# Performance work log

Hardware: AMD Instinct MI355X
Metric: run time of the kernel (lower is better)

Reference implementation:

```python
import jax, jax.numpy as jnp
import numpy as np

# ---- config (mirrors AAModel init kwargs: ns=48, nv=10, sh_lmax=1) ----
N, E, NS, NV = 100000, 60000, 48, 10
SED, DED = 32, 32          # sigma / distance embedding dims
CUTOFF = 30.0              # GaussianSmearing(0, cutoff, DED)
SQ3 = float(np.sqrt(3.0))
W1_NUMEL = NS * NS + NS * NV                                   # 2784
# layer-2 fully-connected TP path weight offsets:
#   0e(x)0e->0e, 0e(x)1o->1o, 1o(x)0e->1o, 1o(x)1o->0e, 1o(x)1o->1e
O2 = [2304, 2784, 2884, 3364, 3464]


def _mlp2(x, W1, b1, W2, b2):
    return jax.nn.relu(x @ W1 + b1) @ W2 + b2


def _seg_mean(x, idx, n):
    s = jax.ops.segment_sum(x, idx, num_segments=n)
    cnt = jax.ops.segment_sum(jnp.ones(idx.shape, x.dtype), idx, num_segments=n)
    return s / jnp.maximum(cnt, 1.0).reshape((n,) + (1,) * (x.ndim - 1))


def _forward(pos, node_sigma_emb, node_s, edge_W1, edge_b1, edge_W2, edge_b2,
             fc1_W1, fc1_b1, fc1_W2, fc1_b2, fc2_W1, fc2_b1, fc2_W2, fc2_b2,
             edge_index):
    src, dst = edge_index[0], edge_index[1]
    vec = pos[dst] - pos[src]                          # [E,3]
    d = jnp.linalg.norm(vec, axis=-1)                  # [E]
    sh1 = SQ3 * vec / (d[:, None] + 1e-8)              # l=1 SH, component norm; sh0 == 1
    # Gaussian smearing of edge distances
    offsets = jnp.linspace(0.0, CUTOFF, DED)
    coeff = -0.5 / (offsets[1] - offsets[0]) ** 2
    demb = jnp.exp(coeff * (d[:, None] - offsets) ** 2)          # [E,DED]
    edge_emb = _mlp2(jnp.concatenate([node_sigma_emb[src], demb], -1),
                     edge_W1, edge_b1, edge_W2, edge_b2)         # [E,NS]

    # ---- conv layer 1:  ns x0e  (x)  1x0e+1x1o  ->  ns x0e + nv x1o ----
    xs = node_s[src]
    ea = jnp.concatenate([edge_emb, node_s[src], node_s[dst]], -1)   # [E,3*NS]
    w = _mlp2(ea, fc1_W1, fc1_b1, fc1_W2, fc1_b2)                    # [E,2784]
    w00 = w[:, :NS * NS].reshape(-1, NS, NS)
    w01 = w[:, NS * NS:].reshape(-1, NS, NV)
    inv = 1.0 / np.sqrt(NS)
    m_s = jnp.einsum('eio,ei->eo', w00, xs) * inv                    # [E,NS]
    m_v = jnp.einsum('eio,ei->eo', w01, xs)[:, :, None] * sh1[:, None, :] * inv  # [E,NV,3]
    node_s1 = node_s + _seg_mean(m_s, dst, N)                        # residual
    node_v1 = _seg_mean(m_v, dst, N)

    # ---- conv layer 2:  ns x0e + nv x1o  (x)  1x0e+1x1o  ->  ns x0e + nv x1o + nv x1e ----
    ea2 = jnp.concatenate([edge_emb, node_s1[src], node_s1[dst]], -1)
    w2 = _mlp2(ea2, fc2_W1, fc2_b1, fc2_W2, fc2_b2)                  # [E,3464]
    w00 = w2[:, :O2[0]].reshape(-1, NS, NS)
    w01 = w2[:, O2[0]:O2[1]].reshape(-1, NS, NV)
    w10 = w2[:, O2[1]:O2[2]].reshape(-1, NV, NV)
    w11s = w2[:, O2[2]:O2[3]].reshape(-1, NV, NS)
    w11p = w2[:, O2[3]:O2[4]].reshape(-1, NV, NV)
    xs, xv = node_s1[src], node_v1[src]
    nA = 1.0 / np.sqrt(2 * NS)
    nB = 1.0 / np.sqrt(2 * NV)
    m_s = (jnp.einsum('eio,ei->eo', w00, xs) * nA
           + jnp.einsum('eio,eid,ed->eo', w11s, xv, sh1) * (nB / SQ3))
    m_v = (jnp.einsum('eio,ei->eo', w01, xs)[:, :, None] * sh1[:, None, :] * nA
           + jnp.einsum('eio,eid->eod', w10, xv) * nB)
    m_p = jnp.einsum('eio,eid->eod', w11p, jnp.cross(xv, sh1[:, None, :])) * (1.0 / np.sqrt(2.0 * NV))
    node_s2 = node_s1 + _seg_mean(m_s, dst, N)
    node_v2 = node_v1 + _seg_mean(m_v, dst, N)
    node_p = _seg_mean(m_p, dst, N)
    # final node irreps ns x0e + nv x1o + nv x1e, flattened -> [N, 108]
    return jnp.concatenate([node_s2, node_v2.reshape(N, -1), node_p.reshape(N, -1)], -1)


def setup_inputs() -> dict:
    key = jax.random.key(0)
    k = jax.random.split(key, 10)
    f32 = jnp.float32
    def lin(kk, fi, fo):
        return jax.random.normal(kk, (fi, fo), f32) / np.sqrt(fi)
    return {
        'pos': 10.0 * jax.random.normal(k[0], (N, 3), f32),
        'node_sigma_emb': jax.random.normal(k[1], (N, SED), f32),
        'node_s': jax.random.normal(k[2], (N, NS), f32),
        'edge_W1': lin(k[3], SED + DED, NS), 'edge_b1': jnp.zeros((NS,), f32),
        'edge_W2': lin(k[4], NS, NS), 'edge_b2': jnp.zeros((NS,), f32),
        'fc1_W1': lin(k[5], 3 * NS, 3 * NS), 'fc1_b1': jnp.zeros((3 * NS,), f32),
        'fc1_W2': lin(k[6], 3 * NS, W1_NUMEL), 'fc1_b2': jnp.zeros((W1_NUMEL,), f32),
        'fc2_W1': lin(k[7], 3 * NS, 3 * NS), 'fc2_b1': jnp.zeros((3 * NS,), f32),
        'fc2_W2': lin(k[8], 3 * NS, O2[-1]), 'fc2_b2': jnp.zeros((O2[-1],), f32),
        'edge_index': jax.random.randint(k[9], (2, E), 0, N, jnp.int32),
    }


def reference(pos, node_sigma_emb, node_s, edge_W1, edge_b1, edge_W2, edge_b2,
              fc1_W1, fc1_b1, fc1_W2, fc1_b2, fc2_W1, fc2_b1, fc2_W2, fc2_b2,
              edge_index):
    return _forward(pos, node_sigma_emb, node_s, edge_W1, edge_b1, edge_W2, edge_b2,
                    fc1_W1, fc1_b1, fc1_W2, fc1_b2, fc2_W1, fc2_b1, fc2_W2, fc2_b2,
                    edge_index)
```

## Files before the change

### kernel.cpp

```cpp
#include <hip/hip_runtime.h>
#include <math.h>


constexpr float SQ3f = 1.7320508075688772f;
constexpr float INV1 = 0.14433756729740643f;
constexpr float NAc  = 0.10206207261596575f;
constexpr float NBc  = 0.22360679774997896f;
constexpr float C20  = 0.22360679774997896f;
constexpr float RATIO= 1.2649110640673518f;
constexpr float DSP  = 30.0f/31.0f;
constexpr float GCOEF= -0.5f/(DSP*DSP);

typedef __attribute__((ext_vector_type(8))) short bf16x8;
typedef __attribute__((ext_vector_type(4))) float f32x4;

__device__ __forceinline__ unsigned short f2bf(float x) {
    unsigned u = __builtin_bit_cast(unsigned, x);
    u += 0x7fffu + ((u >> 16) & 1u);
    return (unsigned short)(u >> 16);
}
__device__ __forceinline__ float bf2f(unsigned short h) {
    return __builtin_bit_cast(float, ((unsigned)h) << 16);
}

__device__ __forceinline__ int colmap(int layer, int t, int lm) {
    if (layer == 0) return t*16 + lm;
    if (layer == 1) {
        if (t < 144) { const int og=t/48, i=t-og*48; return i*48 + og*16 + lm; }
        const int i = t-144; return (lm<10) ? 2304 + i*10 + lm : -1;
    }
    if (t < 144) { const int og=t/48, i=t-og*48; return i*48 + og*16 + lm; }
    if (t < 174) { const int s=t-144, og=s/10, i=s-og*10; return 2884 + i*48 + og*16 + lm; }
    if (t < 222) { const int i=t-174; return (lm<10) ? 2304 + i*10 + lm : -1; }
    if (t < 232) { const int i=t-222; return (lm<10) ? 2784 + i*10 + lm : -1; }
    { const int i=t-232; return (lm<10) ? 3364 + i*10 + lm : -1; }
}

__global__ __launch_bounds__(256)
void cvt_swz(const float* __restrict__ W, const float* __restrict__ bias,
             short* __restrict__ Wsw, int ncol, int ntile, int layer)
{
    const int gid = blockIdx.x*256 + threadIdx.x;
    const int g = gid >> 6, lane = gid & 63;
    if (g >= ntile*5) return;
    const int tile = g/5, ks = g - tile*5;
    const int c  = colmap(layer, tile, lane & 15);
    const int k0 = ks*32 + (lane >> 4)*8;
    union { uint4 u4; unsigned short h[8]; } pk;
    #pragma unroll
    for (int j=0;j<8;j++) {
        const int k = k0 + j;
        float v = 0.f;
        if (c >= 0) {
            if (k < 144)       v = W[(size_t)k*ncol + c];
            else if (k == 144) v = bias[c];
        }
        pk.h[j] = f2bf(v);
    }
    *(uint4*)&Wsw[((size_t)g*64 + lane)*8] = pk.u4;
}

__global__ __launch_bounds__(256)
void edge_kernel(const float* __restrict__ pos, const float* __restrict__ sigma,
                 const int* __restrict__ ei,
                 const float* __restrict__ W1, const float* __restrict__ b1,
                 const float* __restrict__ W2, const float* __restrict__ b2,
                 float* __restrict__ edge_emb, float* __restrict__ sh1buf,
                 int* __restrict__ deg, int E)
{
    __shared__ float inl[4][64];
    __shared__ float hidl[4][48];
    const int w    = threadIdx.x >> 6;
    const int lane = threadIdx.x & 63;
    const int e    = blockIdx.x*4 + w;
    const bool valid = (e < E);
    const int ec = valid ? e : 0;
    const int src = ei[ec], dst = ei[E+ec];
    const float vx = pos[dst*3+0]-pos[src*3+0];
    const float vy = pos[dst*3+1]-pos[src*3+1];
    const float vz = pos[dst*3+2]-pos[src*3+2];
    const float d  = sqrtf(vx*vx+vy*vy+vz*vz);
    const float si = SQ3f/(d+1e-8f);
    const float s0 = vx*si, s1 = vy*si, s2 = vz*si;
    if (lane < 32) {
        inl[w][lane] = sigma[src*32+lane];
    } else {
        const float off  = (float)(lane-32)*DSP;
        const float diff = d - off;
        inl[w][lane] = expf(GCOEF*diff*diff);
    }
    __syncthreads();
    if (lane < 48) {
        float a = b1[lane];
        #pragma unroll 8
        for (int j=0;j<64;j++) a = fmaf(inl[w][j], W1[j*48+lane], a);
        hidl[w][lane] = fmaxf(a, 0.f);
    }
    __syncthreads();
    if (valid) {
        if (lane < 48) {
            float a = b2[lane];
            #pragma unroll 8
            for (int j=0;j<48;j++) a = fmaf(hidl[w][j], W2[j*48+lane], a);
            edge_emb[e*48+lane] = a;
        }
        if (lane == 0) atomicAdd(&deg[dst], 1);
        if (lane < 3)  sh1buf[e*4+lane] = (lane==0)?s0:((lane==1)?s1:s2);
    }
}

__device__ __forceinline__ void load_bfrag(const short* __restrict__ Wsw,
                                           int tile, int lane, bf16x8 (&b)[5]) {
    #pragma unroll
    for (int ks=0; ks<5; ks++)
        b[ks] = *(const bf16x8*)&Wsw[((size_t)(tile*5+ks)*64 + lane)*8];
}

template<int LAYER>
__global__ __launch_bounds__(256)
void conv_kernel(const float* __restrict__ edge_emb, const float* __restrict__ sh1buf,
                 const int* __restrict__ ei,
                 const float* __restrict__ sin_, const float* __restrict__ vin,
                 const short* __restrict__ W1sw, const short* __restrict__ W2sw,
                 float* __restrict__ outS, float* __restrict__ outV, int E)
{
    constexpr int NT = (LAYER==1) ? 192 : 242;
    constexpr int NG = NT/2;

    __shared__ __align__(16) short pool[64*192];
    __shared__ __align__(16) unsigned short xsTb[48][64];
    __shared__ float sh1l[64][4];
    __shared__ int   srcl[64], dstl[64];
    __shared__ __align__(16) float xvT[LAYER==2 ? 30 : 1][64];
    __shared__ __align__(16) float uT [LAYER==2 ? 10 : 1][64];
    __shared__ __align__(16) float cvT[LAYER==2 ? 30 : 1][64];

    const int t  = threadIdx.x;
    const int eb = blockIdx.x * 64;

    if (t < 64) {
        const int ge = eb + t; const int gc = (ge < E) ? ge : (E-1);
        srcl[t] = ei[gc]; dstl[t] = ei[E+gc];
    }
    {
        const int e = t >> 2, k = t & 3;
        const int ge = eb + e; const int gc = (ge<E)?ge:(E-1);
        sh1l[e][k] = sh1buf[gc*4 + k];
    }
    __syncthreads();

    for (int p = t; p < 64*24; p += 256) {
        const int m = p / 24, s = p - m*24;
        const int k0 = s*8;
        float vals[8] = {0.f,0.f,0.f,0.f,0.f,0.f,0.f,0.f};
        if (k0 < 48) {
            const int ge = eb + m; const int gc = (ge<E)?ge:(E-1);
            const float4 a = *(const float4*)&edge_emb[gc*48 + k0];
            const float4 b = *(const float4*)&edge_emb[gc*48 + k0 + 4];
            vals[0]=a.x; vals[1]=a.y; vals[2]=a.z; vals[3]=a.w;
            vals[4]=b.x; vals[5]=b.y; vals[6]=b.z; vals[7]=b.w;
        } else if (k0 < 96) {
            const float4 a = *(const float4*)&sin_[srcl[m]*48 + (k0-48)];
            const float4 b = *(const float4*)&sin_[srcl[m]*48 + (k0-48) + 4];
            vals[0]=a.x; vals[1]=a.y; vals[2]=a.z; vals[3]=a.w;
            vals[4]=b.x; vals[5]=b.y; vals[6]=b.z; vals[7]=b.w;
        } else if (k0 < 144) {
            const float4 a = *(const float4*)&sin_[dstl[m]*48 + (k0-96)];
            const float4 b = *(const float4*)&sin_[dstl[m]*48 + (k0-96) + 4];
            vals[0]=a.x; vals[1]=a.y; vals[2]=a.z; vals[3]=a.w;
            vals[4]=b.x; vals[5]=b.y; vals[6]=b.z; vals[7]=b.w;
        } else if (k0 == 144) {
            vals[0] = 1.f;
        }
        union { uint4 u4; unsigned short h[8]; } pk;
        #pragma unroll
        for (int j=0;j<8;j++) pk.h[j] = f2bf(vals[j]);
        *(uint4*)&pool[m*192 + ((s ^ (m&7))*8)] = pk.u4;
        if (k0 >= 48 && k0 < 96) {
            #pragma unroll
            for (int j=0;j<8;j++) xsTb[k0-48+j][m] = pk.h[j];
        }
    }
    if (LAYER==2) {
        for (int p=t; p<640; p+=256) {
            const int i = p >> 6, e = p & 63;
            const float x0 = vin[srcl[e]*30 + i*3+0];
            const float x1 = vin[srcl[e]*30 + i*3+1];
            const float x2 = vin[srcl[e]*30 + i*3+2];
            const float h0=sh1l[e][0], h1=sh1l[e][1], h2=sh1l[e][2];
            xvT[i*3+0][e]=x0; xvT[i*3+1][e]=x1; xvT[i*3+2][e]=x2;
            uT[i][e] = x0*h0 + x1*h1 + x2*h2;
            cvT[i*3+0][e] = x1*h2 - x2*h1;
            cvT[i*3+1][e] = x2*h0 - x0*h2;
            cvT[i*3+2][e] = x0*h1 - x1*h0;
        }
    }
    __syncthreads();

    const int wv = t >> 6, lane = t & 63;
    const int lm = lane & 15, lk = lane >> 4, lk4 = lk*4;

    f32x4 aa[3][2], ab[3][2];
    {
        bf16x8 af[2][5];
        #pragma unroll
        for (int mt=0; mt<2; mt++) {
            const int m = mt*16 + lm;
            #pragma unroll
            for (int ks=0; ks<5; ks++)
                af[mt][ks] = *(const bf16x8*)&pool[m*192 + (((ks*4+lk) ^ (m&7))*8)];
        }
        #pragma unroll
        for (int j=0; j<3; j++) {
            const int nt = wv + j*4;
            if (nt < 9) {
                bf16x8 bw[5];
                load_bfrag(W1sw, nt, lane, bw);
                #pragma unroll
                for (int mt=0; mt<2; mt++) aa[j][mt] = (f32x4){0.f,0.f,0.f,0.f};
                #pragma unroll
                for (int ks=0; ks<5; ks++)
                    #pragma unroll
                    for (int mt=0; mt<2; mt++)
                        aa[j][mt] = __builtin_amdgcn_mfma_f32_16x16x32_bf16(af[mt][ks], bw[ks], aa[j][mt], 0,0,0);
            }
        }
        #pragma unroll
        for (int mt=0; mt<2; mt++) {
            const int m = (mt+2)*16 + lm;
            #pragma unroll
            for (int ks=0; ks<5; ks++)
                af[mt][ks] = *(const bf16x8*)&pool[m*192 + (((ks*4+lk) ^ (m&7))*8)];
        }
        #pragma unroll
        for (int j=0; j<3; j++) {
            const int nt = wv + j*4;
            if (nt < 9) {
                bf16x8 bw[5];
                load_bfrag(W1sw, nt, lane, bw);
                #pragma unroll
                for (int mt=0; mt<2; mt++) ab[j][mt] = (f32x4){0.f,0.f,0.f,0.f};
                #pragma unroll
                for (int ks=0; ks<5; ks++)
                    #pragma unroll
                    for (int mt=0; mt<2; mt++)
                        ab[j][mt] = __builtin_amdgcn_mfma_f32_16x16x32_bf16(af[mt][ks], bw[ks], ab[j][mt], 0,0,0);
            }
        }
    }
    __syncthreads();
    #pragma unroll
    for (int j=0; j<3; j++) {
        const int nt = wv + j*4;
        if (nt < 9) {
            const int c = nt*16 + lm;
            #pragma unroll
            for (int mt=0; mt<4; mt++) {
                const f32x4 v = (mt<2) ? aa[j][mt] : ab[j][mt-2];
                #pragma unroll
                for (int r=0; r<4; r++) {
                    const int m = mt*16 + lk4 + r;
                    pool[m*192 + (((c>>3) ^ (m&7))*8) + (c&7)] = (short)f2bf(fmaxf(v[r], 0.f));
                }
            }
        }
    }
    if (t < 128) {
        const int m = t >> 1, s = 18 + (t & 1);
        union { uint4 u4; unsigned short h[8]; } pk;
        pk.u4.x = pk.u4.y = pk.u4.z = pk.u4.w = 0u;
        if (s == 18) pk.h[0] = f2bf(1.f);
        *(uint4*)&pool[m*192 + ((s ^ (m&7))*8)] = pk.u4;
    }
    __syncthreads();

    bf16x8 ag[5];
    {
        const int m = wv*16 + lm;
        #pragma unroll
        for (int ks=0; ks<5; ks++)
            ag[ks] = *(const bf16x8*)&pool[m*192 + (((ks*4+lk) ^ (m&7))*8)];
    }
    __syncthreads();

    auto STAGE = [&](int bufsel, int g) {
        const char* gsrc = (const char*)W2sw + (size_t)g*10240;
        char* lbase = (char*)pool + bufsel*10240;
        for (int c = wv; c < 10; c += 4) {
            __builtin_amdgcn_global_load_lds(
                (const __attribute__((address_space(1))) void*)(gsrc + c*1024 + lane*16),
                (__attribute__((address_space(3))) void*)(lbase + c*1024),
                16, 0, 0);
        }
    };

    int gstage = 1, cur = 0;
    STAGE(0, 0);
    __syncthreads();

    const int col0 = wv*16 + lk4;

    auto runpairs = [&](int count, auto&& upd) {
        for (int i = 0; i < count; i += 2) {
            if (gstage < NG) { STAGE(cur^1, gstage); ++gstage; }
            const short* tb = pool + cur*5120;
            #pragma unroll
            for (int s = 0; s < 2; ++s) {
                bf16x8 bf_[5];
                #pragma unroll
                for (int ks=0; ks<5; ks++)
                    bf_[ks] = *(const bf16x8*)&tb[s*2560 + ks*512 + lane*8];
                f32x4 a = (f32x4){0.f,0.f,0.f,0.f};
                #pragma unroll
                for (int ks=0; ks<5; ks++)
                    a = __builtin_amdgcn_mfma_f32_16x16x32_bf16(ag[ks], bf_[ks], a, 0,0,0);
                upd(i+s, a);
            }
            __syncthreads();
            cur ^= 1;
        }
    };

    float ms0[4]={0,0,0,0}, ms1[4]={0,0,0,0}, ms2[4]={0,0,0,0}, vc[4]={0,0,0,0};
    float m3[4][3] = {};
    float p3[4][3] = {};

    auto upd_ms = [&](float (&ms)[4], int i, const f32x4& a, float scale) {
        const ushort4 xw = *(const ushort4*)&xsTb[i][col0];
        ms[0] = fmaf(a[0]*scale, bf2f(xw.x), ms[0]);
        ms[1] = fmaf(a[1]*scale, bf2f(xw.y), ms[1]);
        ms[2] = fmaf(a[2]*scale, bf2f(xw.z), ms[2]);
        ms[3] = fmaf(a[3]*scale, bf2f(xw.w), ms[3]);
    };

    runpairs(48, [&](int i, const f32x4& a){ upd_ms(ms0, i, a, 1.f); });
    runpairs(48, [&](int i, const f32x4& a){ upd_ms(ms1, i, a, 1.f); });
    runpairs(48, [&](int i, const f32x4& a){ upd_ms(ms2, i, a, 1.f); });
    if (LAYER==2) {
        runpairs(10, [&](int i, const f32x4& a){
            const f32x4 u = *(const f32x4*)&uT[i][col0];
            #pragma unroll
            for (int r=0;r<4;r++) ms0[r] = fmaf(a[r]*RATIO, u[r], ms0[r]);
        });
        runpairs(10, [&](int i, const f32x4& a){
            const f32x4 u = *(const f32x4*)&uT[i][col0];
            #pragma unroll
            for (int r=0;r<4;r++) ms1[r] = fmaf(a[r]*RATIO, u[r], ms1[r]);
        });
        runpairs(10, [&](int i, const f32x4& a){
            const f32x4 u = *(const f32x4*)&uT[i][col0];
            #pragma unroll
            for (int r=0;r<4;r++) ms2[r] = fmaf(a[r]*RATIO, u[r], ms2[r]);
        });
    }
    runpairs(48, [&](int i, const f32x4& a){ upd_ms(vc, i, a, 1.f); });
    if (LAYER==2) {
        runpairs(10, [&](int i, const f32x4& a){
            #pragma unroll
            for (int d=0; d<3; d++) {
                const f32x4 x = *(const f32x4*)&xvT[i*3+d][col0];
                #pragma unroll
                for (int r=0;r<4;r++) m3[r][d] = fmaf(a[r], x[r], m3[r][d]);
            }
        });
        runpairs(10, [&](int i, const f32x4& a){
            #pragma unroll
            for (int d=0; d<3; d++) {
                const f32x4 x = *(const f32x4*)&cvT[i*3+d][col0];
                #pragma unroll
                for (int r=0;r<4;r++) p3[r][d] = fmaf(a[r], x[r], p3[r][d]);
            }
        });
    }

    const float sScale = (LAYER==1) ? INV1 : NAc;
    const int   sStrd  = (LAYER==1) ? 48 : 108;
    #pragma unroll
    for (int r=0;r<4;r++) {
        const int e = wv*16 + lk4 + r;
        if (eb+e < E) {
            const size_t base = (size_t)dstl[e]*sStrd;
            unsafeAtomicAdd(&outS[base + 0*16 + lm], ms0[r]*sScale);
            unsafeAtomicAdd(&outS[base + 1*16 + lm], ms1[r]*sScale);
            unsafeAtomicAdd(&outS[base + 2*16 + lm], ms2[r]*sScale);
        }
    }
    if (lm < 10) {
        #pragma unroll
        for (int r=0;r<4;r++) {
            const int e = wv*16 + lk4 + r;
            if (eb+e < E) {
                if (LAYER==1) {
                    const float v = vc[r]*INV1;
                    #pragma unroll
                    for (int d=0; d<3; d++)
                        unsafeAtomicAdd(&outV[(size_t)dstl[e]*30 + lm*3 + d], v*sh1l[e][d]);
                } else {
                    const float v = vc[r]*NAc;
                    const size_t base = (size_t)dstl[e]*108;
                    #pragma unroll
                    for (int d=0; d<3; d++) {
                        unsafeAtomicAdd(&outS[base + 48 + lm*3 + d], v*sh1l[e][d] + m3[r][d]*NBc);
                        unsafeAtomicAdd(&outS[base + 78 + lm*3 + d], p3[r][d]*C20);
                    }
                }
            }
        }
    }
}

__global__ __launch_bounds__(256)
void fin1_kernel(const float* __restrict__ node_s, const int* __restrict__ deg,
                 float* __restrict__ s1, float* __restrict__ v1, int Nn)
{
    const int p = blockIdx.x*256 + threadIdx.x;
    const int totS = Nn*48;
    if (p < totS) {
        const int n = p/48;
        const int dgi = deg[n];
        const float dg = (float)(dgi > 1 ? dgi : 1);
        s1[p] = node_s[p] + s1[p]/dg;
    } else {
        const int q = p - totS;
        if (q < Nn*30) {
            const int n = q/30;
            const int dgi = deg[n];
            const float dg = (float)(dgi > 1 ? dgi : 1);
            v1[q] = v1[q]/dg;
        }
    }
}

__global__ __launch_bounds__(256)
void fin2_kernel(const float* __restrict__ s1, const float* __restrict__ v1,
                 const int* __restrict__ deg, float* __restrict__ out, int Nn)
{
    const int p = blockIdx.x*256 + threadIdx.x;
    if (p >= Nn*108) return;
    const int n = p/108, c = p - n*108;
    const int dgi = deg[n];
    const float dg = (float)(dgi > 1 ? dgi : 1);
    const float acc = out[p]/dg;
    if (c < 48)      out[p] = s1[n*48+c] + acc;
    else if (c < 78) out[p] = v1[n*30 + (c-48)] + acc;
    else             out[p] = acc;
}

extern "C" void kernel_launch(void* const* d_in, const int* in_sizes, int n_in,
                              void* d_out, int out_size, void* d_ws, size_t ws_size,
                              hipStream_t stream)
{
    const float* pos    = (const float*)d_in[0];
    const float* sigma  = (const float*)d_in[1];
    const float* node_s = (const float*)d_in[2];
    const float* eW1  = (const float*)d_in[3];
    const float* eb1  = (const float*)d_in[4];
    const float* eW2  = (const float*)d_in[5];
    const float* eb2  = (const float*)d_in[6];
    const float* f1W1 = (const float*)d_in[7];
    const float* f1b1 = (const float*)d_in[8];
    const float* f1W2 = (const float*)d_in[9];
    const float* f1b2 = (const float*)d_in[10];
    const float* f2W1 = (const float*)d_in[11];
    const float* f2b1 = (const float*)d_in[12];
    const float* f2W2 = (const float*)d_in[13];
    const float* f2b2 = (const float*)d_in[14];
    const int*   ei   = (const int*)d_in[15];
    const int Nn = in_sizes[0]/3;
    const int E  = in_sizes[15]/2;
    float* out = (float*)d_out;

    char* ws = (char*)d_ws;
    float* edge_emb = (float*)ws;  ws += (size_t)E*48*sizeof(float);
    float* sh1buf   = (float*)ws;  ws += (size_t)E*4*sizeof(float);
    float* s1       = (float*)ws;  ws += (size_t)Nn*48*sizeof(float);
    float* v1       = (float*)ws;  ws += (size_t)Nn*30*sizeof(float);
    int*   deg      = (int*)ws;    ws += (size_t)Nn*sizeof(int);
    short* W1sw     = (short*)ws;  ws += (size_t)9*5*64*8*sizeof(short);
    short* W2sw     = (short*)ws;  ws += (size_t)242*5*64*8*sizeof(short);

    hipMemsetAsync(s1,  0, (size_t)Nn*48*sizeof(float), stream);
    hipMemsetAsync(v1,  0, (size_t)Nn*30*sizeof(float), stream);
    hipMemsetAsync(deg, 0, (size_t)Nn*sizeof(int),      stream);
    hipMemsetAsync(out, 0, (size_t)Nn*108*sizeof(float), stream);

    edge_kernel<<<(E+3)/4, 256, 0, stream>>>(pos, sigma, ei, eW1, eb1, eW2, eb2,
                                             edge_emb, sh1buf, deg, E);

    cvt_swz<<<(9*5*64+255)/256,   256, 0, stream>>>(f1W1, f1b1, W1sw, 144, 9, 0);
    cvt_swz<<<(192*5*64+255)/256, 256, 0, stream>>>(f1W2, f1b2, W2sw, 2784, 192, 1);

    conv_kernel<1><<<(E+63)/64, 256, 0, stream>>>(edge_emb, sh1buf, ei, node_s, nullptr,
                                                  W1sw, W2sw, s1, v1, E);
    fin1_kernel<<<((size_t)Nn*78 + 255)/256, 256, 0, stream>>>(node_s, deg, s1, v1, Nn);

    cvt_swz<<<(9*5*64+255)/256,   256, 0, stream>>>(f2W1, f2b1, W1sw, 144, 9, 0);
    cvt_swz<<<(242*5*64+255)/256, 256, 0, stream>>>(f2W2, f2b2, W2sw, 3464, 242, 2);

    conv_kernel<2><<<(E+63)/64, 256, 0, stream>>>(edge_emb, sh1buf, ei, s1, v1,
                                                  W1sw, W2sw, out, nullptr, E);
    fin2_kernel<<<((size_t)Nn*108 + 255)/256, 256, 0, stream>>>(s1, v1, deg, out, Nn);
}
```

Baseline: 494.5 us.

## Replace atomic scatter-mean with CSR-based per-node gather of edge messages

Conv kernels now write per-edge messages to a dense buffer instead of atomically adding into node accumulators. A degree scan and a placement kernel build a dst-sorted CSR edge list, and gather kernels sum each node's messages, divide by degree and add the residual. This removes float atomics and several memsets. In exchange it adds a single-block scan, an atomic placement pass, an extra E*108 message buffer write/read, and irregular gather reads.

New measurement: 697.6 us. +41.1%, slower.

```diff
diff --git a/kernel.cpp b/kernel.cpp
--- a/kernel.cpp
+++ b/kernel.cpp
@@ -109,6 +109,43 @@
     }
 }
 
+__global__ __launch_bounds__(1024)
+void scan_kernel(const int* __restrict__ deg, int* __restrict__ rowptr,
+                 int* __restrict__ cursor, int Nn)
+{
+    __shared__ int part[1024];
+    const int t = threadIdx.x;
+    const int chunk = (Nn + 1023)/1024;
+    const int base = t*chunk;
+    int s = 0;
+    for (int i=0;i<chunk;i++) { const int n=base+i; if (n<Nn) s += deg[n]; }
+    part[t] = s;
+    __syncthreads();
+    for (int off=1; off<1024; off<<=1) {
+        const int v = (t>=off) ? part[t-off] : 0;
+        __syncthreads();
+        part[t] += v;
+        __syncthreads();
+    }
+    int run = part[t] - s;
+    for (int i=0;i<chunk;i++) {
+        const int n=base+i;
+        if (n<Nn) { rowptr[n]=run; cursor[n]=run; run += deg[n]; }
+    }
+    if (t==0) rowptr[Nn] = part[1023];
+}
+
+__global__ __launch_bounds__(256)
+void place_kernel(const int* __restrict__ ei, int* __restrict__ cursor,
+                  int* __restrict__ csr, int E)
+{
+    const int e = blockIdx.x*256 + threadIdx.x;
+    if (e >= E) return;
+    const int dst = ei[E+e];
+    const int slot = atomicAdd(&cursor[dst], 1);
+    csr[slot] = e;
+}
+
 __device__ __forceinline__ void load_bfrag(const short* __restrict__ Wsw,
                                            int tile, int lane, bf16x8 (&b)[5]) {
     #pragma unroll
@@ -122,10 +159,11 @@
                  const int* __restrict__ ei,
                  const float* __restrict__ sin_, const float* __restrict__ vin,
                  const short* __restrict__ W1sw, const short* __restrict__ W2sw,
-                 float* __restrict__ outS, float* __restrict__ outV, int E)
+                 float* __restrict__ msg, int E)
 {
     constexpr int NT = (LAYER==1) ? 192 : 242;
     constexpr int NG = NT/2;
+    constexpr int ST = (LAYER==1) ? 78 : 108;
 
     __shared__ __align__(16) short pool[64*192];
     __shared__ __align__(16) unsigned short xsTb[48][64];
@@ -374,34 +412,35 @@
     }
 
     const float sScale = (LAYER==1) ? INV1 : NAc;
-    const int   sStrd  = (LAYER==1) ? 48 : 108;
     #pragma unroll
     for (int r=0;r<4;r++) {
         const int e = wv*16 + lk4 + r;
-        if (eb+e < E) {
-            const size_t base = (size_t)dstl[e]*sStrd;
-            unsafeAtomicAdd(&outS[base + 0*16 + lm], ms0[r]*sScale);
-            unsafeAtomicAdd(&outS[base + 1*16 + lm], ms1[r]*sScale);
-            unsafeAtomicAdd(&outS[base + 2*16 + lm], ms2[r]*sScale);
+        const int ge = eb + e;
+        if (ge < E) {
+            float* mb = msg + (size_t)ge*ST;
+            mb[0*16 + lm] = ms0[r]*sScale;
+            mb[1*16 + lm] = ms1[r]*sScale;
+            mb[2*16 + lm] = ms2[r]*sScale;
         }
     }
     if (lm < 10) {
         #pragma unroll
         for (int r=0;r<4;r++) {
             const int e = wv*16 + lk4 + r;
-            if (eb+e < E) {
+            const int ge = eb + e;
+            if (ge < E) {
+                float* mb = msg + (size_t)ge*ST;
                 if (LAYER==1) {
                     const float v = vc[r]*INV1;
                     #pragma unroll
                     for (int d=0; d<3; d++)
-                        unsafeAtomicAdd(&outV[(size_t)dstl[e]*30 + lm*3 + d], v*sh1l[e][d]);
+                        mb[48 + lm*3 + d] = v*sh1l[e][d];
                 } else {
                     const float v = vc[r]*NAc;
-                    const size_t base = (size_t)dstl[e]*108;
                     #pragma unroll
                     for (int d=0; d<3; d++) {
-                        unsafeAtomicAdd(&outS[base + 48 + lm*3 + d], v*sh1l[e][d] + m3[r][d]*NBc);
-                        unsafeAtomicAdd(&outS[base + 78 + lm*3 + d], p3[r][d]*C20);
+                        mb[48 + lm*3 + d] = v*sh1l[e][d] + m3[r][d]*NBc;
+                        mb[78 + lm*3 + d] = p3[r][d]*C20;
                     }
                 }
             }
@@ -410,40 +449,41 @@
 }
 
 __global__ __launch_bounds__(256)
-void fin1_kernel(const float* __restrict__ node_s, const int* __restrict__ deg,
-                 float* __restrict__ s1, float* __restrict__ v1, int Nn)
+void gather1_kernel(const float* __restrict__ node_s, const float* __restrict__ msg,
+                    const int* __restrict__ rowptr, const int* __restrict__ csr,
+                    float* __restrict__ s1, float* __restrict__ v1, int Nn)
 {
     const int p = blockIdx.x*256 + threadIdx.x;
-    const int totS = Nn*48;
-    if (p < totS) {
-        const int n = p/48;
-        const int dgi = deg[n];
-        const float dg = (float)(dgi > 1 ? dgi : 1);
-        s1[p] = node_s[p] + s1[p]/dg;
-    } else {
-        const int q = p - totS;
-        if (q < Nn*30) {
-            const int n = q/30;
-            const int dgi = deg[n];
-            const float dg = (float)(dgi > 1 ? dgi : 1);
-            v1[q] = v1[q]/dg;
-        }
-    }
+    if (p >= Nn*78) return;
+    const int n = p/78, c = p - n*78;
+    const int r0 = rowptr[n], r1 = rowptr[n+1];
+    float s = 0.f;
+    for (int j=r0; j<r1; j++) s += msg[(size_t)csr[j]*78 + c];
+    const int dgi = r1 - r0;
+    s /= (float)(dgi > 1 ? dgi : 1);
+    if (c < 48) s1[n*48 + c] = node_s[n*48 + c] + s;
+    else        v1[n*30 + (c-48)] = s;
 }
 
 __global__ __launch_bounds__(256)
-void fin2_kernel(const float* __restrict__ s1, const float* __restrict__ v1,
-                 const int* __restrict__ deg, float* __restrict__ out, int Nn)
+void gather2_kernel(const float* __restrict__ s1, const float* __restrict__ v1,
+                    const float* __restrict__ msg,
+                    const int* __restrict__ rowptr, const int* __restrict__ csr,
+                    float* __restrict__ out, int Nn)
 {
     const int p = blockIdx.x*256 + threadIdx.x;
     if (p >= Nn*108) return;
     const int n = p/108, c = p - n*108;
-    const int dgi = deg[n];
-    const float dg = (float)(dgi > 1 ? dgi : 1);
-    const float acc = out[p]/dg;
-    if (c < 48)      out[p] = s1[n*48+c] + acc;
-    else if (c < 78) out[p] = v1[n*30 + (c-48)] + acc;
-    else             out[p] = acc;
+    const int r0 = rowptr[n], r1 = rowptr[n+1];
+    float s = 0.f;
+    for (int j=r0; j<r1; j++) s += msg[(size_t)csr[j]*108 + c];
+    const int dgi = r1 - r0;
+    s /= (float)(dgi > 1 ? dgi : 1);
+    float base;
+    if (c < 48)      base = s1[n*48 + c];
+    else if (c < 78) base = v1[n*30 + (c-48)];
+    else             base = 0.f;
+    out[p] = base + s;
 }
 
 extern "C" void kernel_launch(void* const* d_in, const int* in_sizes, int n_in,
@@ -476,28 +516,33 @@
     float* s1       = (float*)ws;  ws += (size_t)Nn*48*sizeof(float);
     float* v1       = (float*)ws;  ws += (size_t)Nn*30*sizeof(float);
     int*   deg      = (int*)ws;    ws += (size_t)Nn*sizeof(int);
+    int*   rowptr   = (int*)ws;    ws += (size_t)(Nn+1)*sizeof(int);
+    int*   cursor   = (int*)ws;    ws += (size_t)Nn*sizeof(int);
+    int*   csr      = (int*)ws;    ws += (size_t)E*sizeof(int);
     short* W1sw     = (short*)ws;  ws += (size_t)9*5*64*8*sizeof(short);
     short* W2sw     = (short*)ws;  ws += (size_t)242*5*64*8*sizeof(short);
-
-    hipMemsetAsync(s1,  0, (size_t)Nn*48*sizeof(float), stream);
-    hipMemsetAsync(v1,  0, (size_t)Nn*30*sizeof(float), stream);
-    hipMemsetAsync(deg, 0, (size_t)Nn*sizeof(int),      stream);
-    hipMemsetAsync(out, 0, (size_t)Nn*108*sizeof(float), stream);
+    float* msg      = (float*)ws;  ws += (size_t)E*108*sizeof(float);
+
+    hipMemsetAsync(deg, 0, (size_t)Nn*sizeof(int), stream);
 
     edge_kernel<<<(E+3)/4, 256, 0, stream>>>(pos, sigma, ei, eW1, eb1, eW2, eb2,
                                              edge_emb, sh1buf, deg, E);
+    scan_kernel<<<1, 1024, 0, stream>>>(deg, rowptr, cursor, Nn);
+    place_kernel<<<(E+255)/256, 256, 0, stream>>>(ei, cursor, csr, E);
 
     cvt_swz<<<(9*5*64+255)/256,   256, 0, stream>>>(f1W1, f1b1, W1sw, 144, 9, 0);
     cvt_swz<<<(192*5*64+255)/256, 256, 0, stream>>>(f1W2, f1b2, W2sw, 2784, 192, 1);
 
     conv_kernel<1><<<(E+63)/64, 256, 0, stream>>>(edge_emb, sh1buf, ei, node_s, nullptr,
-                                                  W1sw, W2sw, s1, v1, E);
-    fin1_kernel<<<((size_t)Nn*78 + 255)/256, 256, 0, stream>>>(node_s, deg, s1, v1, Nn);
+                                                  W1sw, W2sw, msg, E);
+    gather1_kernel<<<((size_t)Nn*78 + 255)/256, 256, 0, stream>>>(node_s, msg, rowptr, csr,
+                                                                  s1, v1, Nn);
 
     cvt_swz<<<(9*5*64+255)/256,   256, 0, stream>>>(f2W1, f2b1, W1sw, 144, 9, 0);
     cvt_swz<<<(242*5*64+255)/256, 256, 0, stream>>>(f2W2, f2b2, W2sw, 3464, 242, 2);
 
     conv_kernel<2><<<(E+63)/64, 256, 0, stream>>>(edge_emb, sh1buf, ei, s1, v1,
-                                                  W1sw, W2sw, out, nullptr, E);
-    fin2_kernel<<<((size_t)Nn*108 + 255)/256, 256, 0, stream>>>(s1, v1, deg, out, Nn);
-}
+                                                  W1sw, W2sw, msg, E);
+    gather2_kernel<<<((size_t)Nn*108 + 255)/256, 256, 0, stream>>>(s1, v1, msg, rowptr, csr,
+                                                                   out, Nn);
+}
```
